# Optimization experiments

Measured on AMD Instinct MI355X. Metric: run time of the kernel, lower is better.

The kernel has to match this reference:

```python
import jax, jax.numpy as jnp
import numpy as np


def setup_inputs() -> dict:
    key = jax.random.key(0)
    kx, kw = jax.random.split(key)
    x = jax.random.normal(kx, (32, 256, 56, 56), dtype=jnp.float32)
    # kaiming-uniform-like init for weights [O, I, K, K]
    fan_in = 256 * 3 * 3
    bound = float(np.sqrt(6.0 / fan_in))
    weights = jax.random.uniform(kw, (256, 256, 3, 3), dtype=jnp.float32,
                                 minval=-bound, maxval=bound)
    return {"x": x, "weights": weights}


def reference(x, weights):
    # Binarize weights with sign (STE is a backward-only concern; forward uses sign).
    qw = jnp.sign(weights)
    # conv2d, NCHW / OIHW, stride 1, no padding, no bias
    out = jax.lax.conv_general_dilated(
        x, qw,
        window_strides=(1, 1),
        padding="VALID",
        dimension_numbers=("NCHW", "OIHW", "NCHW"),
    )
    return out
```

## Files before the change

### kernel.cpp

```cpp
#include <hip/hip_runtime.h>
#include <cstdint>

#define NB 32
#define IC 256
#define OC 256
#define H 56
#define WIDTH 56
#define OH 54
#define OW 54
#define HW (H*WIDTH)
#define OHW (OH*OW)
#define KTOT 2304
#define M_TOT (NB*OHW)
#define C8N (IC/8)

#define BM 96
#define BO 256
#define BK 32
#define KSTEPS (KTOT/BK)
#define MBLOCKS (M_TOT/BM)
#define XBLK ((NB*C8N*HW)/256)

__device__ __align__(16) unsigned short g_qwt[KSTEPS*BO*BK];
__device__ __align__(16) unsigned short g_xq[NB*C8N*HW*8];

typedef __bf16 bf16x8 __attribute__((ext_vector_type(8)));
typedef float  f32x4  __attribute__((ext_vector_type(4)));

typedef __attribute__((address_space(1))) const unsigned int gas_u32;
typedef __attribute__((address_space(3))) unsigned int las_u32;
__device__ __forceinline__ void async_copy16(const void* g, void* l) {
  __builtin_amdgcn_global_load_lds((gas_u32*)g, (las_u32*)l, 16, 0, 0);
}

__device__ inline unsigned short f32_bf16(float f) {
  union { float f; unsigned int u; } v; v.f = f;
  unsigned int u = v.u;
  return (unsigned short)((u + 0x7FFFu + ((u >> 16) & 1u)) >> 16);
}

#define WAITV(N) asm volatile("s_waitcnt vmcnt(" #N ")" ::: "memory")
#define BARRIER() do { \
  __builtin_amdgcn_sched_barrier(0); \
  __builtin_amdgcn_s_barrier(); \
  __builtin_amdgcn_sched_barrier(0); \
} while (0)

__global__ __launch_bounds__(256) void prep(const float* __restrict__ x,
                                            const float* __restrict__ w) {
  const int t = threadIdx.x;
  if (blockIdx.x < XBLK) {
    int g = blockIdx.x * 256 + t;
    int hw = g % HW;
    int tc = g / HW;
    int c8 = tc & 31;
    int n  = tc >> 5;
    const float* src = x + (n*IC + c8*8)*HW + hw;
    unsigned int o[4];
    #pragma unroll
    for (int j = 0; j < 4; ++j) {
      unsigned int lo = f32_bf16(src[(2*j+0)*HW]);
      unsigned int hi = f32_bf16(src[(2*j+1)*HW]);
      o[j] = lo | (hi << 16);
    }
    *(uint4*)(&g_xq[g*8]) = *(uint4*)o;
  } else {
    int L = (blockIdx.x - XBLK) * 256 + t;
    int step = L >> 13;
    int r    = (L >> 5) & 255;
    int kc   = L & 31;
    int cs   = kc >> 3;
    int b    = kc & 7;
    int csrc = cs ^ ((r >> 1) & 3);
    int k    = step*BK + csrc*8 + b;
    int pos  = k >> 8;
    int c    = k & 255;
    float v = w[r*2304 + c*9 + pos];
    g_qwt[L] = (v > 0.f) ? 0x3F80u : ((v < 0.f) ? 0xBF80u : 0u);
  }
}

__global__ __launch_bounds__(512) void bconv_gemm(float* __restrict__ out) {
  __shared__ __align__(16) unsigned short Wl[2][BO*BK + 2560];
  __shared__ __align__(16) unsigned short Xl[2][BM*BK];
  const int t = threadIdx.x;

  const int orig = blockIdx.x;
  const int xcd  = orig & 7;
  const int idx  = orig >> 3;
  const int base = (xcd < 4) ? xcd*122 : (4*122 + (xcd - 4)*121);
  const int bm   = base + idx;
  const int m0   = bm * BM;

  int xbase;
  {
    const int i   = (t >> 2) % 96;
    const int cs  = t & 3;
    const int csw = cs ^ ((i >> 1) & 3);
    int m  = m0 + i;
    int n  = m / OHW;
    int rm = m - n*OHW;
    int oh = rm / OW;
    int ow = rm - oh*OW;
    xbase = ((n*C8N + csw)*HW + oh*WIDTH + ow) * 8;
  }

  const int lane = t & 63;
  const int wv   = t >> 6;
  const int col  = lane & 15;
  const int quad = lane >> 4;
  const int wo   = (wv >> 1) * 64;
  const int wm   = (wv & 1) * 48;
  const int sw   = (quad ^ ((col >> 1) & 3)) * 8;
  int aoff[4], boff[3];
  #pragma unroll
  for (int i = 0; i < 4; ++i)
    aoff[i] = (wo + i*16 + col)*BK + sw;
  #pragma unroll
  for (int i = 0; i < 3; ++i)
    boff[i] = (wm + i*16 + col)*BK + sw;

  auto STAGE = [&](int step, int buf) {
    const unsigned short* ws = g_qwt + step*(BO*BK);
    async_copy16(&ws[t*8],       &Wl[buf][t*8]);
    async_copy16(&ws[(t+512)*8], &Wl[buf][(t+512)*8]);
    if (t < 384) {
      const int pos = step >> 3;
      const int kh  = pos / 3;
      const int kw  = pos - kh*3;
      const int xo  = xbase + (((step & 7)*4)*HW + kh*WIDTH + kw)*8;
      async_copy16(&g_xq[xo], &Xl[buf][t*8]);
    } else {
      async_copy16(&ws[t*8], &Wl[buf][t*8]);
    }
  };

  f32x4 acc[4][3];
  #pragma unroll
  for (int a = 0; a < 4; ++a)
    #pragma unroll
    for (int b = 0; b < 3; ++b)
      acc[a][b] = (f32x4){0.f, 0.f, 0.f, 0.f};

  auto COMPUTE = [&](const unsigned short* Wb, const unsigned short* Xb) {
    bf16x8 av[4], bv[3];
    #pragma unroll
    for (int i = 0; i < 4; ++i) av[i] = *(const bf16x8*)(&Wb[aoff[i]]);
    #pragma unroll
    for (int i = 0; i < 3; ++i) bv[i] = *(const bf16x8*)(&Xb[boff[i]]);
    __builtin_amdgcn_s_setprio(1);
    #pragma unroll
    for (int io = 0; io < 4; ++io)
      #pragma unroll
      for (int im = 0; im < 3; ++im)
        acc[io][im] = __builtin_amdgcn_mfma_f32_16x16x32_bf16(av[io], bv[im], acc[io][im], 0, 0, 0);
    __builtin_amdgcn_s_setprio(0);
  };

  STAGE(0, 0);
  STAGE(1, 1);
  WAITV(3);
  BARRIER();

  #pragma unroll 1
  for (int s = 0; s < 70; s += 2) {
    COMPUTE(Wl[0], Xl[0]);
    BARRIER();
    STAGE(s + 2, 0);
    WAITV(3);
    BARRIER();

    COMPUTE(Wl[1], Xl[1]);
    BARRIER();
    STAGE(s + 3, 1);
    WAITV(3);
    BARRIER();
  }

  COMPUTE(Wl[0], Xl[0]);
  WAITV(0);
  BARRIER();
  COMPUTE(Wl[1], Xl[1]);

  #pragma unroll
  for (int im = 0; im < 3; ++im) {
    int m  = m0 + wm + im*16 + col;
    int n  = m / OHW;
    int rm = m - n*OHW;
    float* obase = out + n*(OC*OHW) + rm;
    #pragma unroll
    for (int io = 0; io < 4; ++io) {
      int orow = wo + io*16 + quad*4;
      #pragma unroll
      for (int r = 0; r < 4; ++r)
        obase[(orow + r)*OHW] = acc[io][im][r];
    }
  }
}

extern "C" void kernel_launch(void* const* d_in, const int* in_sizes, int n_in,
                              void* d_out, int out_size, void* d_ws, size_t ws_size,
                              hipStream_t stream) {
  const float* x = (const float*)d_in[0];
  const float* w = (const float*)d_in[1];
  float* out = (float*)d_out;

  prep<<<dim3(XBLK + (KSTEPS*BO*BK)/256), 256, 0, stream>>>(x, w);
  bconv_gemm<<<dim3(MBLOCKS), 512, 0, stream>>>(out);
}
```

Measured before the change: 305.0 us.

## Load activations straight into registers and triple-buffer weights in LDS

The activation tile no longer goes through LDS. Each wave loads its bf16x8 activation fragments straight from global memory into registers, two steps ahead, while weight tiles rotate through three LDS buffers. The explicit vmcnt waits inside the main loop are gone. Ordering now relies on the in-order completion of the register loads, which implies the earlier async weight copies have landed before each barrier. Launch bounds now request two blocks per CU. The aim is to cut LDS traffic and barrier count, at the cost of redundant global/L1 activation loads across waves and tighter register pressure.

```diff
diff --git a/kernel.cpp b/kernel.cpp
--- a/kernel.cpp
+++ b/kernel.cpp
@@ -20,6 +20,7 @@
 #define KSTEPS (KTOT/BK)
 #define MBLOCKS (M_TOT/BM)
 #define XBLK ((NB*C8N*HW)/256)
+#define WPAD 1024
 
 __device__ __align__(16) unsigned short g_qwt[KSTEPS*BO*BK];
 __device__ __align__(16) unsigned short g_xq[NB*C8N*HW*8];
@@ -40,11 +41,8 @@
 }
 
 #define WAITV(N) asm volatile("s_waitcnt vmcnt(" #N ")" ::: "memory")
-#define BARRIER() do { \
-  __builtin_amdgcn_sched_barrier(0); \
-  __builtin_amdgcn_s_barrier(); \
-  __builtin_amdgcn_sched_barrier(0); \
-} while (0)
+#define SCHEDB() __builtin_amdgcn_sched_barrier(0)
+#define BARRIER() do { SCHEDB(); __builtin_amdgcn_s_barrier(); SCHEDB(); } while (0)
 
 __global__ __launch_bounds__(256) void prep(const float* __restrict__ x,
                                             const float* __restrict__ w) {
@@ -80,30 +78,15 @@
   }
 }
 
-__global__ __launch_bounds__(512) void bconv_gemm(float* __restrict__ out) {
-  __shared__ __align__(16) unsigned short Wl[2][BO*BK + 2560];
-  __shared__ __align__(16) unsigned short Xl[2][BM*BK];
+__global__ __launch_bounds__(512, 2) void bconv_gemm(float* __restrict__ out) {
+  __shared__ __align__(16) unsigned short Wl[3][BO*BK + WPAD];
   const int t = threadIdx.x;
 
   const int orig = blockIdx.x;
   const int xcd  = orig & 7;
   const int idx  = orig >> 3;
   const int base = (xcd < 4) ? xcd*122 : (4*122 + (xcd - 4)*121);
-  const int bm   = base + idx;
-  const int m0   = bm * BM;
-
-  int xbase;
-  {
-    const int i   = (t >> 2) % 96;
-    const int cs  = t & 3;
-    const int csw = cs ^ ((i >> 1) & 3);
-    int m  = m0 + i;
-    int n  = m / OHW;
-    int rm = m - n*OHW;
-    int oh = rm / OW;
-    int ow = rm - oh*OW;
-    xbase = ((n*C8N + csw)*HW + oh*WIDTH + ow) * 8;
-  }
+  const int m0   = (base + idx) * BM;
 
   const int lane = t & 63;
   const int wv   = t >> 6;
@@ -112,28 +95,25 @@
   const int wo   = (wv >> 1) * 64;
   const int wm   = (wv & 1) * 48;
   const int sw   = (quad ^ ((col >> 1) & 3)) * 8;
-  int aoff[4], boff[3];
+  int aoff[4];
   #pragma unroll
   for (int i = 0; i < 4; ++i)
     aoff[i] = (wo + i*16 + col)*BK + sw;
-  #pragma unroll
-  for (int i = 0; i < 3; ++i)
-    boff[i] = (wm + i*16 + col)*BK + sw;
-
-  auto STAGE = [&](int step, int buf) {
-    const unsigned short* ws = g_qwt + step*(BO*BK);
-    async_copy16(&ws[t*8],       &Wl[buf][t*8]);
-    async_copy16(&ws[(t+512)*8], &Wl[buf][(t+512)*8]);
-    if (t < 384) {
-      const int pos = step >> 3;
-      const int kh  = pos / 3;
-      const int kw  = pos - kh*3;
-      const int xo  = xbase + (((step & 7)*4)*HW + kh*WIDTH + kw)*8;
-      async_copy16(&g_xq[xo], &Xl[buf][t*8]);
-    } else {
-      async_copy16(&ws[t*8], &Wl[buf][t*8]);
+
+  int pbq0, pbq1, pbq2;
+  {
+    int pb[3];
+    #pragma unroll
+    for (int i = 0; i < 3; ++i) {
+      int m  = m0 + wm + i*16 + col;
+      int n  = m / OHW;
+      int rm = m - n*OHW;
+      int oh = rm / OW;
+      int ow = rm - oh*OW;
+      pb[i] = ((n*C8N + quad)*HW + oh*WIDTH + ow) * 8;
     }
-  };
+    pbq0 = pb[0]; pbq1 = pb[1]; pbq2 = pb[2];
+  }
 
   f32x4 acc[4][3];
   #pragma unroll
@@ -142,45 +122,84 @@
     for (int b = 0; b < 3; ++b)
       acc[a][b] = (f32x4){0.f, 0.f, 0.f, 0.f};
 
-  auto COMPUTE = [&](const unsigned short* Wb, const unsigned short* Xb) {
-    bf16x8 av[4], bv[3];
-    #pragma unroll
-    for (int i = 0; i < 4; ++i) av[i] = *(const bf16x8*)(&Wb[aoff[i]]);
-    #pragma unroll
-    for (int i = 0; i < 3; ++i) bv[i] = *(const bf16x8*)(&Xb[boff[i]]);
-    __builtin_amdgcn_s_setprio(1);
-    #pragma unroll
-    for (int io = 0; io < 4; ++io)
-      #pragma unroll
-      for (int im = 0; im < 3; ++im)
-        acc[io][im] = __builtin_amdgcn_mfma_f32_16x16x32_bf16(av[io], bv[im], acc[io][im], 0, 0, 0);
-    __builtin_amdgcn_s_setprio(0);
-  };
-
-  STAGE(0, 0);
-  STAGE(1, 1);
-  WAITV(3);
+  bf16x8 xa0, xa1, xa2, xb0, xb1, xb2;
+
+#define STAGE_W(step, WBUF) do { \
+    const unsigned short* ws_ = g_qwt + (step)*(BO*BK); \
+    async_copy16(&ws_[t*8],       &WBUF[t*8]); \
+    async_copy16(&ws_[(t+512)*8], &WBUF[(t+512)*8]); \
+  } while (0)
+
+#define LOADX(step, X0, X1, X2) do { \
+    int pos_ = (step) >> 3; \
+    int kh_  = pos_ / 3; \
+    int kw_  = pos_ - 3*kh_; \
+    int sA_  = ((((step)*4) & 31)*HW + kh_*WIDTH + kw_) * 8; \
+    X0 = *(const bf16x8*)(&g_xq[pbq0 + sA_]); \
+    X1 = *(const bf16x8*)(&g_xq[pbq1 + sA_]); \
+    X2 = *(const bf16x8*)(&g_xq[pbq2 + sA_]); \
+  } while (0)
+
+#define COMPUTEM(WB, X0, X1, X2) do { \
+    bf16x8 av_[4]; \
+    _Pragma("unroll") \
+    for (int i = 0; i < 4; ++i) av_[i] = *(const bf16x8*)(&WB[aoff[i]]); \
+    __builtin_amdgcn_s_setprio(1); \
+    _Pragma("unroll") \
+    for (int io = 0; io < 4; ++io) { \
+      acc[io][0] = __builtin_amdgcn_mfma_f32_16x16x32_bf16(av_[io], X0, acc[io][0], 0, 0, 0); \
+      acc[io][1] = __builtin_amdgcn_mfma_f32_16x16x32_bf16(av_[io], X1, acc[io][1], 0, 0, 0); \
+      acc[io][2] = __builtin_amdgcn_mfma_f32_16x16x32_bf16(av_[io], X2, acc[io][2], 0, 0, 0); \
+    } \
+    __builtin_amdgcn_s_setprio(0); \
+  } while (0)
+
+#define PHASE(p_, WB, CX0, CX1, CX2) do { \
+    COMPUTEM(WB, CX0, CX1, CX2); \
+    BARRIER(); \
+    STAGE_W((p_) + 3, WB); \
+    SCHEDB(); \
+    LOADX((p_) + 2, CX0, CX1, CX2); \
+    SCHEDB(); \
+  } while (0)
+
+  STAGE_W(0, Wl[0]);
+  STAGE_W(1, Wl[1]);
+  SCHEDB();
+  LOADX(0, xa0, xa1, xa2);
+  SCHEDB();
+  STAGE_W(2, Wl[2]);
+  SCHEDB();
+  LOADX(1, xb0, xb1, xb2);
+  SCHEDB();
+  WAITV(10);
   BARRIER();
 
   #pragma unroll 1
-  for (int s = 0; s < 70; s += 2) {
-    COMPUTE(Wl[0], Xl[0]);
-    BARRIER();
-    STAGE(s + 2, 0);
-    WAITV(3);
-    BARRIER();
-
-    COMPUTE(Wl[1], Xl[1]);
-    BARRIER();
-    STAGE(s + 3, 1);
-    WAITV(3);
-    BARRIER();
-  }
-
-  COMPUTE(Wl[0], Xl[0]);
-  WAITV(0);
+  for (int s = 0; s < 66; s += 6) {
+    PHASE(s + 0, Wl[0], xa0, xa1, xa2);
+    PHASE(s + 1, Wl[1], xb0, xb1, xb2);
+    PHASE(s + 2, Wl[2], xa0, xa1, xa2);
+    PHASE(s + 3, Wl[0], xb0, xb1, xb2);
+    PHASE(s + 4, Wl[1], xa0, xa1, xa2);
+    PHASE(s + 5, Wl[2], xb0, xb1, xb2);
+  }
+
+  PHASE(66, Wl[0], xa0, xa1, xa2);
+  PHASE(67, Wl[1], xb0, xb1, xb2);
+  PHASE(68, Wl[2], xa0, xa1, xa2);
+  COMPUTEM(Wl[0], xb0, xb1, xb2);
   BARRIER();
-  COMPUTE(Wl[1], Xl[1]);
+  LOADX(71, xb0, xb1, xb2);
+  SCHEDB();
+  COMPUTEM(Wl[1], xa0, xa1, xa2);
+  BARRIER();
+  COMPUTEM(Wl[2], xb0, xb1, xb2);
+
+#undef PHASE
+#undef COMPUTEM
+#undef LOADX
+#undef STAGE_W
 
   #pragma unroll
   for (int im = 0; im < 3; ++im) {
```

Result: slower. 314.7 us (+3.2%).
